# Kernel tuning notes

Measured on AMD Instinct MI355X. Metric: run time of the kernel, lower is better.

## Reference

```python
import jax, jax.numpy as jnp
import numpy as np

N_NODES = 50000
N_EDGES = 1_600_000
F_IN = 32
HIDDEN = 32
HORIZON = 12
K = 2


def setup_inputs() -> dict:
    key = jax.random.key(0)
    ks = jax.random.split(key, 12)
    s = 0.1  # keep gates away from saturation
    x = jax.random.normal(ks[0], (N_NODES, 1, F_IN), dtype=jnp.float32)
    edge_index = jax.random.randint(ks[1], (2, N_EDGES), 0, N_NODES, dtype=jnp.int64)
    edge_weight = jax.random.uniform(ks[2], (N_EDGES,), dtype=jnp.float32)
    Wx = jax.random.normal(ks[3], (4, K, F_IN, HIDDEN), dtype=jnp.float32) * s
    bx = jax.random.normal(ks[4], (4, HIDDEN), dtype=jnp.float32) * s
    Wh = jax.random.normal(ks[5], (4, K, HIDDEN, HIDDEN), dtype=jnp.float32) * s
    bh = jax.random.normal(ks[6], (4, HIDDEN), dtype=jnp.float32) * s
    wc = jax.random.normal(ks[7], (3, HIDDEN), dtype=jnp.float32) * s
    b = jax.random.normal(ks[8], (4, HIDDEN), dtype=jnp.float32) * s
    W_lin = jax.random.normal(ks[9], (HIDDEN, HORIZON), dtype=jnp.float32) * s
    b_lin = jax.random.normal(ks[10], (HORIZON,), dtype=jnp.float32) * s
    h0 = jnp.zeros((N_NODES, HIDDEN), dtype=jnp.float32)
    c0 = jnp.zeros((N_NODES, HIDDEN), dtype=jnp.float32)
    return dict(x=x, edge_index=edge_index, edge_weight=edge_weight, Wx=Wx, bx=bx,
                Wh=Wh, bh=bh, wc=wc, b=b, W_lin=W_lin, b_lin=b_lin, h0=h0, c0=c0)


def reference(x, edge_index, edge_weight, Wx, bx, Wh, bh, wc, b, W_lin, b_lin, h0, c0):
    N = x.shape[0]
    src, dst = edge_index[0], edge_index[1]
    # ChebConv sym normalization with lambda_max=2: L_hat = L - I = -D^{-1/2} A D^{-1/2}
    deg = jax.ops.segment_sum(edge_weight, src, num_segments=N)
    dinv = jnp.where(deg > 0, jax.lax.rsqrt(deg), 0.0)
    nw = -dinv[src] * edge_weight * dinv[dst]  # [E]

    X = x[:, 0, :]  # squeeze(1) -> [N, F]

    def cheb(Z, W, bb):
        # K=2 Chebyshev: T0(Z)=Z, T1(Z)=L_hat Z (sparse gather-scatter)
        LZ = jax.ops.segment_sum(nw[:, None] * Z[src], dst, num_segments=N)
        return Z @ W[0] + LZ @ W[1] + bb

    # gate order: i, f, c, o
    I = jax.nn.sigmoid(cheb(X, Wx[0], bx[0]) + cheb(h0, Wh[0], bh[0]) + wc[0] * c0 + b[0])
    Fg = jax.nn.sigmoid(cheb(X, Wx[1], bx[1]) + cheb(h0, Wh[1], bh[1]) + wc[1] * c0 + b[1])
    T = jnp.tanh(cheb(X, Wx[2], bx[2]) + cheb(h0, Wh[2], bh[2]) + b[2])
    C = Fg * c0 + I * T
    O = jax.nn.sigmoid(cheb(X, Wx[3], bx[3]) + cheb(h0, Wh[3], bh[3]) + wc[2] * C + b[3])
    H = O * jnp.tanh(C)

    h = jax.nn.relu(H) @ W_lin + b_lin  # Linear(32, horizon)
    return (h, H, C)
```

## Files before the change

### kernel.cpp

```cpp
#include <hip/hip_runtime.h>
#include <math.h>

#define HID 32
#define HOR 12
#define NB 256
#define NPT 4

__device__ __forceinline__ float sigmoidf_(float x) { return 1.0f / (1.0f + expf(-x)); }


__global__ __launch_bounds__(256) void k_hist(const int* __restrict__ src,
                                              const int* __restrict__ dst,
                                              int* __restrict__ hist,
                                              int E, int chunk, int ng) {
    __shared__ int hS[256], hD[256];
    int t = threadIdx.x, b = blockIdx.x;
    hS[t] = 0; hD[t] = 0;
    __syncthreads();
    int beg = b * chunk, end = min(E, beg + chunk);
    for (int e = beg + t; e < end; e += 256) {
        atomicAdd(&hS[src[e] >> 8], 1);
        atomicAdd(&hD[dst[e] >> 8], 1);
    }
    __syncthreads();
    if (t < ng) {
        hist[(size_t)t * NB + b] = hS[t];
        hist[((size_t)ng + t) * NB + b] = hD[t];
    }
}

__global__ __launch_bounds__(256) void k_binscan(const int* __restrict__ hist,
                                                 int* __restrict__ off,
                                                 int* __restrict__ binTot, int ng) {
    __shared__ int s[256];
    int b2 = blockIdx.x, t = threadIdx.x;
    int v = hist[(size_t)b2 * NB + t];
    s[t] = v;
    __syncthreads();
    for (int o = 1; o < 256; o <<= 1) {
        int x = (t >= o) ? s[t - o] : 0;
        __syncthreads();
        s[t] += x;
        __syncthreads();
    }
    off[(size_t)b2 * NB + t] = s[t] - v;
    if (t == 255) {
        int idx = (b2 < ng) ? b2 : 256 + (b2 - ng);
        binTot[idx] = s[255];
    }
}

__global__ __launch_bounds__(512) void k_binbase(const int* __restrict__ binTot,
                                                 int* __restrict__ baseS, int* __restrict__ baseD,
                                                 int* __restrict__ rowptr,
                                                 int E, int ng, int N) {
    __shared__ int buf[512];
    int t = threadIdx.x;
    int lt = t & 255;
    int sum = (lt < ng) ? binTot[(t < 256 ? 0 : 256) + lt] : 0;
    buf[t] = sum;
    __syncthreads();
    for (int o = 1; o < 256; o <<= 1) {
        int v = (lt >= o) ? buf[t - o] : 0;
        __syncthreads();
        buf[t] += v;
        __syncthreads();
    }
    int base = buf[t] - sum;
    if (lt < ng) { if (t < 256) baseS[lt] = base; else baseD[lt] = base; }
    if (t == 0)   { baseS[ng] = E; rowptr[N] = E; }
    if (t == 256) { baseD[ng] = E; }
}

__global__ __launch_bounds__(256) void k_scatter(const int* __restrict__ src,
                                                 const int* __restrict__ dst,
                                                 const float* __restrict__ w,
                                                 const int* __restrict__ off,
                                                 const int* __restrict__ baseS,
                                                 const int* __restrict__ baseD,
                                                 int2* __restrict__ tmpS, int2* __restrict__ tmpD,
                                                 int E, int chunk, int ng) {
    __shared__ int cS[256], cD[256];
    int t = threadIdx.x, b = blockIdx.x;
    if (t < ng) {
        cS[t] = off[(size_t)t * NB + b] + baseS[t];
        cD[t] = off[((size_t)ng + t) * NB + b] + baseD[t];
    }
    __syncthreads();
    int beg = b * chunk, end = min(E, beg + chunk);
    for (int e = beg + t; e < end; e += 256) {
        int s = src[e], d = dst[e];
        int wb = __float_as_int(w[e]);
        int pS = atomicAdd(&cS[s >> 8], 1);
        tmpS[pS] = make_int2(s, wb);
        int pD = atomicAdd(&cD[d >> 8], 1);
        tmpD[pD] = make_int2(s | ((d & 255) << 16), wb);
    }
}

__global__ __launch_bounds__(256) void k_degsum(const int2* __restrict__ tmpS,
                                                const int* __restrict__ baseS,
                                                float* __restrict__ dinv, int N) {
    __shared__ float h[256];
    int g = blockIdx.x, t = threadIdx.x;
    h[t] = 0.0f;
    __syncthreads();
    int beg = baseS[g], end = baseS[g + 1];
    for (int i = beg + t; i < end; i += 256) {
        int2 p = tmpS[i];
        atomicAdd(&h[p.x & 255], __int_as_float(p.y));
    }
    __syncthreads();
    int n = (g << 8) + t;
    if (n < N) { float s = h[t]; dinv[n] = (s > 0.0f) ? rsqrtf(s) : 0.0f; }
}

__global__ __launch_bounds__(256) void k_scatter2(const int2* __restrict__ tmpD,
                                                  const int* __restrict__ baseD,
                                                  const float* __restrict__ dinv,
                                                  int* __restrict__ rowptr,
                                                  int2* __restrict__ epair, int N) {
    __shared__ int h[256];
    __shared__ int cur[256];
    int g = blockIdx.x, t = threadIdx.x;
    h[t] = 0;
    __syncthreads();
    int beg = baseD[g], end = baseD[g + 1];
    for (int i = beg + t; i < end; i += 256) atomicAdd(&h[(tmpD[i].x >> 16) & 255], 1);
    __syncthreads();
    int v = h[t];
    for (int off = 1; off < 256; off <<= 1) {
        int x = (t >= off) ? h[t - off] : 0;
        __syncthreads();
        h[t] += x;
        __syncthreads();
    }
    int excl = h[t] - v;
    int n = (g << 8) + t;
    if (n < N) rowptr[n] = beg + excl;
    cur[t] = beg + excl;
    __syncthreads();
    for (int i = beg + t; i < end; i += 256) {
        int2 p = tmpD[i];
        int low = (p.x >> 16) & 255;
        int s = p.x & 0xFFFF;
        int pos = atomicAdd(&cur[low], 1);
        float nw = -dinv[s] * __int_as_float(p.y) * dinv[(g << 8) + low];
        epair[pos] = make_int2(s, __float_as_int(nw));
    }
}

__global__ void k_flags(const float* __restrict__ h0, const float* __restrict__ c0,
                        int* __restrict__ flag, int total) {
    int i = blockIdx.x * 256 + threadIdx.x;
    float a = (i < total) ? h0[i] : 0.0f;
    float c = (i < total) ? c0[i] : 0.0f;
    unsigned long long ba = __ballot(a != 0.0f);
    unsigned long long bc = __ballot(c != 0.0f);
    if ((threadIdx.x & 63) == 0) {
        int m = (ba ? 1 : 0) | (bc ? 2 : 0);
        if (m) atomicOr(flag, m);
    }
}

__global__ __launch_bounds__(256) void k_gather(const int* __restrict__ rowptr,
                                                const int2* __restrict__ epair,
                                                const float* __restrict__ X,
                                                const float* __restrict__ H0,
                                                const int* __restrict__ hflag,
                                                float* __restrict__ LX, float* __restrict__ LH,
                                                int N) {
    int tid = blockIdx.x * 256 + threadIdx.x;
    int n = tid >> 5;
    int f = tid & 31;
    if (n >= N) return;
    int beg = rowptr[n], end = rowptr[n + 1];
    float acc = 0.0f, accH = 0.0f;
    int fl = *hflag;
    if (fl & 1) {
        #pragma unroll 4
        for (int i = beg; i < end; ++i) {
            int2 p = epair[i];
            float w = __int_as_float(p.y);
            acc  += w * X[(p.x << 5) + f];
            accH += w * H0[(p.x << 5) + f];
        }
    } else {
        #pragma unroll 4
        for (int i = beg; i < end; ++i) {
            int2 p = epair[i];
            acc += __int_as_float(p.y) * X[(p.x << 5) + f];
        }
    }
    LX[(n << 5) + f] = acc;
    if (fl & 1) LH[(n << 5) + f] = accH;
}

__global__ __launch_bounds__(256) void k_gates(
    const float* __restrict__ X, const float* __restrict__ LX,
    const float* __restrict__ H0, const float* __restrict__ LH,
    const float* __restrict__ C0,
    const float* __restrict__ Wx, const float* __restrict__ bx,
    const float* __restrict__ Wh, const float* __restrict__ bh,
    const float* __restrict__ wc, const float* __restrict__ b,
    const int* __restrict__ flag,
    float* __restrict__ outH, float* __restrict__ outC, int N) {
    int tid = blockIdx.x * 256 + threadIdx.x;
    int g = tid >> 5;
    int j = tid & 31;
    int n0 = g * NPT;
    if (n0 >= N) return;
    int cnt = min(NPT, N - n0);
    int f2 = *flag;

    if (f2 == 0) {
        float xk[NPT], lxk[NPT];
        #pragma unroll
        for (int i = 0; i < NPT; ++i) { xk[i] = 0.0f; lxk[i] = 0.0f; }
        for (int i = 0; i < cnt; ++i) {
            int base = (n0 + i) << 5;
            xk[i]  = X[base + j];
            lxk[i] = LX[base + j];
        }
        float p0[NPT], p2[NPT], p3[NPT];
        float b0 = bx[0 * HID + j] + bh[0 * HID + j] + b[0 * HID + j];
        float b2 = bx[2 * HID + j] + bh[2 * HID + j] + b[2 * HID + j];
        float b3 = bx[3 * HID + j] + bh[3 * HID + j] + b[3 * HID + j];
        #pragma unroll
        for (int i = 0; i < NPT; ++i) { p0[i] = b0; p2[i] = b2; p3[i] = b3; }

        #pragma unroll 4
        for (int k = 0; k < HID; ++k) {
            int row = k * HID + j;
            float w00 = Wx[0 * 2048 + row], w01 = Wx[0 * 2048 + 1024 + row];
            float w20 = Wx[2 * 2048 + row], w21 = Wx[2 * 2048 + 1024 + row];
            float w30 = Wx[3 * 2048 + row], w31 = Wx[3 * 2048 + 1024 + row];
            #pragma unroll
            for (int i = 0; i < NPT; ++i) {
                float xv  = __shfl(xk[i],  k, 32);
                float lxv = __shfl(lxk[i], k, 32);
                p0[i] += xv * w00 + lxv * w01;
                p2[i] += xv * w20 + lxv * w21;
                p3[i] += xv * w30 + lxv * w31;
            }
        }

        float wc2 = wc[2 * HID + j];
        for (int i = 0; i < cnt; ++i) {
            int base = (n0 + i) << 5;
            float I = sigmoidf_(p0[i]);
            float T = tanhf(p2[i]);
            float C = I * T;
            float O = sigmoidf_(p3[i] + wc2 * C);
            outH[base + j] = O * tanhf(C);
            outC[base + j] = C;
        }
        return;
    }

    float xk[NPT], lxk[NPT], hk[NPT], lhk[NPT];
    #pragma unroll
    for (int i = 0; i < NPT; ++i) { xk[i] = 0.0f; lxk[i] = 0.0f; hk[i] = 0.0f; lhk[i] = 0.0f; }
    for (int i = 0; i < cnt; ++i) {
        int base = (n0 + i) << 5;
        xk[i]  = X[base + j];
        lxk[i] = LX[base + j];
        hk[i]  = H0[base + j];
        lhk[i] = (f2 & 1) ? LH[base + j] : 0.0f;
    }

    float pre[4][NPT];
    #pragma unroll
    for (int gt = 0; gt < 4; ++gt) {
        float bb = bx[gt * HID + j] + bh[gt * HID + j] + b[gt * HID + j];
        #pragma unroll
        for (int i = 0; i < NPT; ++i) pre[gt][i] = bb;
    }

    #pragma unroll 2
    for (int k = 0; k < HID; ++k) {
        float w0[4], w1[4], w2[4], w3[4];
        int row = k * HID + j;
        #pragma unroll
        for (int gt = 0; gt < 4; ++gt) {
            w0[gt] = Wx[gt * 2048 + row];
            w1[gt] = Wx[gt * 2048 + 1024 + row];
            w2[gt] = Wh[gt * 2048 + row];
            w3[gt] = Wh[gt * 2048 + 1024 + row];
        }
        #pragma unroll
        for (int i = 0; i < NPT; ++i) {
            float xv  = __shfl(xk[i],  k, 32);
            float lxv = __shfl(lxk[i], k, 32);
            float hv  = __shfl(hk[i],  k, 32);
            float lhv = __shfl(lhk[i], k, 32);
            #pragma unroll
            for (int gt = 0; gt < 4; ++gt)
                pre[gt][i] += xv * w0[gt] + lxv * w1[gt] + hv * w2[gt] + lhv * w3[gt];
        }
    }

    float wc0 = wc[0 * HID + j], wc1 = wc[1 * HID + j], wc2 = wc[2 * HID + j];
    for (int i = 0; i < cnt; ++i) {
        int base = (n0 + i) << 5;
        float c0v = C0[base + j];
        float I  = sigmoidf_(pre[0][i] + wc0 * c0v);
        float Fg = sigmoidf_(pre[1][i] + wc1 * c0v);
        float T  = tanhf(pre[2][i]);
        float C  = Fg * c0v + I * T;
        float O  = sigmoidf_(pre[3][i] + wc2 * C);
        float H  = O * tanhf(C);
        outH[base + j] = H;
        outC[base + j] = C;
    }
}

__global__ void k_head(const float* __restrict__ H, const float* __restrict__ Wl,
                       const float* __restrict__ bl, float* __restrict__ hout, int N) {
    int tid = blockIdx.x * 256 + threadIdx.x;
    int n = tid / HOR;
    int t = tid - n * HOR;
    if (n >= N) return;
    float acc = bl[t];
    #pragma unroll
    for (int k = 0; k < HID; ++k) {
        float v = H[(n << 5) + k];
        acc += fmaxf(v, 0.0f) * Wl[k * HOR + t];
    }
    hout[n * HOR + t] = acc;
}

extern "C" void kernel_launch(void* const* d_in, const int* in_sizes, int n_in,
                              void* d_out, int out_size, void* d_ws, size_t ws_size,
                              hipStream_t stream) {
    const float* x  = (const float*)d_in[0];
    const int*   ei = (const int*)d_in[1];
    const float* ew = (const float*)d_in[2];
    const float* Wx = (const float*)d_in[3];
    const float* bx = (const float*)d_in[4];
    const float* Wh = (const float*)d_in[5];
    const float* bh = (const float*)d_in[6];
    const float* wc = (const float*)d_in[7];
    const float* b  = (const float*)d_in[8];
    const float* Wl = (const float*)d_in[9];
    const float* bl = (const float*)d_in[10];
    const float* h0 = (const float*)d_in[11];
    const float* c0 = (const float*)d_in[12];

    int N = in_sizes[0] / HID;
    int E = in_sizes[2];
    const int* src = ei;
    const int* dst = ei + E;

    int ng = (N + 255) >> 8;
    int chunk = (E + NB - 1) / NB;

    int* wsi = (int*)d_ws;
    int2*  tmpD   = (int2*)wsi;
    int2*  tmpS   = (int2*)(wsi + 2 * (size_t)E);
    int2*  epair  = tmpS;
    float* LX     = (float*)(wsi + 4 * (size_t)E);
    float* LH     = LX + (size_t)N * HID;
    int*   rowptr = (int*)(LH + (size_t)N * HID);
    int*   hist   = rowptr + (N + 1);
    int*   off    = hist + 2 * (size_t)ng * NB;
    int*   binTot = off + 2 * (size_t)ng * NB;
    int*   baseS  = binTot + 512;
    int*   baseD  = baseS + 257;
    float* dinv   = (float*)(baseD + 257);
    int*   flag   = (int*)(dinv + N);

    float* hOut = (float*)d_out;
    float* HOut = hOut + (size_t)N * HOR;
    float* COut = HOut + (size_t)N * HID;

    hipMemsetAsync(flag, 0, sizeof(int), stream);

    k_hist<<<NB, 256, 0, stream>>>(src, dst, hist, E, chunk, ng);
    k_binscan<<<2 * ng, 256, 0, stream>>>(hist, off, binTot, ng);
    k_binbase<<<1, 512, 0, stream>>>(binTot, baseS, baseD, rowptr, E, ng, N);
    k_scatter<<<NB, 256, 0, stream>>>(src, dst, ew, off, baseS, baseD, tmpS, tmpD, E, chunk, ng);
    k_degsum<<<ng, 256, 0, stream>>>(tmpS, baseS, dinv, N);
    k_flags<<<(N * HID + 255) / 256, 256, 0, stream>>>(h0, c0, flag, N * HID);
    k_scatter2<<<ng, 256, 0, stream>>>(tmpD, baseD, dinv, rowptr, epair, N);

    k_gather<<<(N * HID + 255) / 256, 256, 0, stream>>>(rowptr, epair, x, h0, flag, LX, LH, N);

    int gThreads = ((N + NPT - 1) / NPT) * 32;
    k_gates<<<(gThreads + 255) / 256, 256, 0, stream>>>(x, LX, h0, LH, c0,
                                                        Wx, bx, Wh, bh, wc, b, flag,
                                                        HOut, COut, N);

    k_head<<<(N * HOR + 255) / 256, 256, 0, stream>>>(HOut, Wl, bl, hOut, N);
}
```

Baseline: 278.4 us.

## Shrink CSR bucket width to 64 nodes and transpose offset layout

Changes the CSR build's coarse bucket size from 256 to 64 nodes, giving about 782 buckets instead of 196. The degree-sum and second-scatter kernels therefore launch four times as many blocks, and each block handles fewer edges. Histogram and scatter blocks grow to 1024 threads, the bin-base scan splits into two 1024-thread blocks, and the offset array is transposed so each scatter block reads its offsets contiguously. The aim is more parallelism and less per-block serial work in the edge sort, at the cost of larger histograms, more shared-memory atomics spread over bins, and mostly idle threads in the 256-thread blocks that now cover only 64 nodes.

Result: no change. 275.5 us (-1.0%).

```diff
diff --git a/kernel.cpp b/kernel.cpp
--- a/kernel.cpp
+++ b/kernel.cpp
@@ -3,35 +3,37 @@
 
 #define HID 32
 #define HOR 12
-#define NB 256
+#define NB  256
+#define GSH 6
+#define GW  64
 #define NPT 4
 
 __device__ __forceinline__ float sigmoidf_(float x) { return 1.0f / (1.0f + expf(-x)); }
 
 
-__global__ __launch_bounds__(256) void k_hist(const int* __restrict__ src,
-                                              const int* __restrict__ dst,
-                                              int* __restrict__ hist,
-                                              int E, int chunk, int ng) {
-    __shared__ int hS[256], hD[256];
+__global__ __launch_bounds__(1024) void k_hist(const int* __restrict__ src,
+                                               const int* __restrict__ dst,
+                                               int* __restrict__ hist,
+                                               int E, int chunk, int ng) {
+    __shared__ int hS[1024], hD[1024];
     int t = threadIdx.x, b = blockIdx.x;
-    hS[t] = 0; hD[t] = 0;
+    for (int i = t; i < ng; i += 1024) { hS[i] = 0; hD[i] = 0; }
     __syncthreads();
     int beg = b * chunk, end = min(E, beg + chunk);
-    for (int e = beg + t; e < end; e += 256) {
-        atomicAdd(&hS[src[e] >> 8], 1);
-        atomicAdd(&hD[dst[e] >> 8], 1);
-    }
-    __syncthreads();
-    if (t < ng) {
-        hist[(size_t)t * NB + b] = hS[t];
-        hist[((size_t)ng + t) * NB + b] = hD[t];
+    for (int e = beg + t; e < end; e += 1024) {
+        atomicAdd(&hS[src[e] >> GSH], 1);
+        atomicAdd(&hD[dst[e] >> GSH], 1);
+    }
+    __syncthreads();
+    for (int i = t; i < ng; i += 1024) {
+        hist[(size_t)i * NB + b] = hS[i];
+        hist[((size_t)ng + i) * NB + b] = hD[i];
     }
 }
 
 __global__ __launch_bounds__(256) void k_binscan(const int* __restrict__ hist,
                                                  int* __restrict__ off,
-                                                 int* __restrict__ binTot, int ng) {
+                                                 int* __restrict__ binTot, int ng2) {
     __shared__ int s[256];
     int b2 = blockIdx.x, t = threadIdx.x;
     int v = hist[(size_t)b2 * NB + t];
@@ -43,76 +45,74 @@
         s[t] += x;
         __syncthreads();
     }
-    off[(size_t)b2 * NB + t] = s[t] - v;
-    if (t == 255) {
-        int idx = (b2 < ng) ? b2 : 256 + (b2 - ng);
-        binTot[idx] = s[255];
-    }
-}
-
-__global__ __launch_bounds__(512) void k_binbase(const int* __restrict__ binTot,
-                                                 int* __restrict__ baseS, int* __restrict__ baseD,
-                                                 int* __restrict__ rowptr,
-                                                 int E, int ng, int N) {
-    __shared__ int buf[512];
+    off[(size_t)t * ng2 + b2] = s[t] - v;
+    if (t == 255) binTot[b2] = s[255];
+}
+
+__global__ __launch_bounds__(1024) void k_binbase(const int* __restrict__ binTot,
+                                                  int* __restrict__ baseS, int* __restrict__ baseD,
+                                                  int* __restrict__ rowptr,
+                                                  int E, int ng, int N) {
+    __shared__ int buf[1024];
     int t = threadIdx.x;
-    int lt = t & 255;
-    int sum = (lt < ng) ? binTot[(t < 256 ? 0 : 256) + lt] : 0;
+    int isD = blockIdx.x;
+    int sum = (t < ng) ? binTot[isD * ng + t] : 0;
     buf[t] = sum;
     __syncthreads();
-    for (int o = 1; o < 256; o <<= 1) {
-        int v = (lt >= o) ? buf[t - o] : 0;
+    for (int o = 1; o < 1024; o <<= 1) {
+        int v = (t >= o) ? buf[t - o] : 0;
         __syncthreads();
         buf[t] += v;
         __syncthreads();
     }
     int base = buf[t] - sum;
-    if (lt < ng) { if (t < 256) baseS[lt] = base; else baseD[lt] = base; }
-    if (t == 0)   { baseS[ng] = E; rowptr[N] = E; }
-    if (t == 256) { baseD[ng] = E; }
-}
-
-__global__ __launch_bounds__(256) void k_scatter(const int* __restrict__ src,
-                                                 const int* __restrict__ dst,
-                                                 const float* __restrict__ w,
-                                                 const int* __restrict__ off,
-                                                 const int* __restrict__ baseS,
-                                                 const int* __restrict__ baseD,
-                                                 int2* __restrict__ tmpS, int2* __restrict__ tmpD,
-                                                 int E, int chunk, int ng) {
-    __shared__ int cS[256], cD[256];
+    int* B = isD ? baseD : baseS;
+    if (t < ng) B[t] = base;
+    if (t == 0) { B[ng] = E; if (!isD) rowptr[N] = E; }
+}
+
+__global__ __launch_bounds__(1024) void k_scatter(const int* __restrict__ src,
+                                                  const int* __restrict__ dst,
+                                                  const float* __restrict__ w,
+                                                  const int* __restrict__ off,
+                                                  const int* __restrict__ baseS,
+                                                  const int* __restrict__ baseD,
+                                                  int2* __restrict__ tmpS, int2* __restrict__ tmpD,
+                                                  int E, int chunk, int ng) {
+    __shared__ int cS[1024], cD[1024];
     int t = threadIdx.x, b = blockIdx.x;
-    if (t < ng) {
-        cS[t] = off[(size_t)t * NB + b] + baseS[t];
-        cD[t] = off[((size_t)ng + t) * NB + b] + baseD[t];
+    int ng2 = 2 * ng;
+    for (int i = t; i < ng; i += 1024) {
+        cS[i] = off[(size_t)b * ng2 + i] + baseS[i];
+        cD[i] = off[(size_t)b * ng2 + ng + i] + baseD[i];
     }
     __syncthreads();
     int beg = b * chunk, end = min(E, beg + chunk);
-    for (int e = beg + t; e < end; e += 256) {
+    for (int e = beg + t; e < end; e += 1024) {
         int s = src[e], d = dst[e];
         int wb = __float_as_int(w[e]);
-        int pS = atomicAdd(&cS[s >> 8], 1);
+        int pS = atomicAdd(&cS[s >> GSH], 1);
         tmpS[pS] = make_int2(s, wb);
-        int pD = atomicAdd(&cD[d >> 8], 1);
-        tmpD[pD] = make_int2(s | ((d & 255) << 16), wb);
+        int pD = atomicAdd(&cD[d >> GSH], 1);
+        tmpD[pD] = make_int2(s | ((d & (GW - 1)) << 16), wb);
     }
 }
 
 __global__ __launch_bounds__(256) void k_degsum(const int2* __restrict__ tmpS,
                                                 const int* __restrict__ baseS,
                                                 float* __restrict__ dinv, int N) {
-    __shared__ float h[256];
+    __shared__ float h[GW];
     int g = blockIdx.x, t = threadIdx.x;
-    h[t] = 0.0f;
+    if (t < GW) h[t] = 0.0f;
     __syncthreads();
     int beg = baseS[g], end = baseS[g + 1];
     for (int i = beg + t; i < end; i += 256) {
         int2 p = tmpS[i];
-        atomicAdd(&h[p.x & 255], __int_as_float(p.y));
-    }
-    __syncthreads();
-    int n = (g << 8) + t;
-    if (n < N) { float s = h[t]; dinv[n] = (s > 0.0f) ? rsqrtf(s) : 0.0f; }
+        atomicAdd(&h[p.x & (GW - 1)], __int_as_float(p.y));
+    }
+    __syncthreads();
+    int n = (g << GSH) + t;
+    if (t < GW && n < N) { float s = h[t]; dinv[n] = (s > 0.0f) ? rsqrtf(s) : 0.0f; }
 }
 
 __global__ __launch_bounds__(256) void k_scatter2(const int2* __restrict__ tmpD,
@@ -120,32 +120,33 @@
                                                   const float* __restrict__ dinv,
                                                   int* __restrict__ rowptr,
                                                   int2* __restrict__ epair, int N) {
-    __shared__ int h[256];
-    __shared__ int cur[256];
+    __shared__ int h[GW], cur[GW];
     int g = blockIdx.x, t = threadIdx.x;
-    h[t] = 0;
+    if (t < GW) h[t] = 0;
     __syncthreads();
     int beg = baseD[g], end = baseD[g + 1];
-    for (int i = beg + t; i < end; i += 256) atomicAdd(&h[(tmpD[i].x >> 16) & 255], 1);
-    __syncthreads();
-    int v = h[t];
-    for (int off = 1; off < 256; off <<= 1) {
-        int x = (t >= off) ? h[t - off] : 0;
-        __syncthreads();
-        h[t] += x;
-        __syncthreads();
-    }
-    int excl = h[t] - v;
-    int n = (g << 8) + t;
-    if (n < N) rowptr[n] = beg + excl;
-    cur[t] = beg + excl;
+    for (int i = beg + t; i < end; i += 256) atomicAdd(&h[(tmpD[i].x >> 16) & (GW - 1)], 1);
+    __syncthreads();
+    int v = (t < GW) ? h[t] : 0;
+    for (int o = 1; o < GW; o <<= 1) {
+        int x = (t < GW && t >= o) ? h[t - o] : 0;
+        __syncthreads();
+        if (t < GW && t >= o) h[t] += x;
+        __syncthreads();
+    }
+    if (t < GW) {
+        int excl = h[t] - v;
+        int n = (g << GSH) + t;
+        if (n < N) rowptr[n] = beg + excl;
+        cur[t] = beg + excl;
+    }
     __syncthreads();
     for (int i = beg + t; i < end; i += 256) {
         int2 p = tmpD[i];
-        int low = (p.x >> 16) & 255;
+        int low = (p.x >> 16) & (GW - 1);
         int s = p.x & 0xFFFF;
         int pos = atomicAdd(&cur[low], 1);
-        float nw = -dinv[s] * __int_as_float(p.y) * dinv[(g << 8) + low];
+        float nw = -dinv[s] * __int_as_float(p.y) * dinv[(g << GSH) + low];
         epair[pos] = make_int2(s, __float_as_int(nw));
     }
 }
@@ -352,7 +353,8 @@
     const int* src = ei;
     const int* dst = ei + E;
 
-    int ng = (N + 255) >> 8;
+    int ng = (N + GW - 1) >> GSH;
+    int ng2 = 2 * ng;
     int chunk = (E + NB - 1) / NB;
 
     int* wsi = (int*)d_ws;
@@ -363,11 +365,11 @@
     float* LH     = LX + (size_t)N * HID;
     int*   rowptr = (int*)(LH + (size_t)N * HID);
     int*   hist   = rowptr + (N + 1);
-    int*   off    = hist + 2 * (size_t)ng * NB;
-    int*   binTot = off + 2 * (size_t)ng * NB;
-    int*   baseS  = binTot + 512;
-    int*   baseD  = baseS + 257;
-    float* dinv   = (float*)(baseD + 257);
+    int*   off    = hist + (size_t)ng2 * NB;
+    int*   binTot = off + (size_t)ng2 * NB;
+    int*   baseS  = binTot + 2048;
+    int*   baseD  = baseS + (ng + 1);
+    float* dinv   = (float*)(baseD + (ng + 1));
     int*   flag   = (int*)(dinv + N);
 
     float* hOut = (float*)d_out;
@@ -376,10 +378,10 @@
 
     hipMemsetAsync(flag, 0, sizeof(int), stream);
 
-    k_hist<<<NB, 256, 0, stream>>>(src, dst, hist, E, chunk, ng);
-    k_binscan<<<2 * ng, 256, 0, stream>>>(hist, off, binTot, ng);
-    k_binbase<<<1, 512, 0, stream>>>(binTot, baseS, baseD, rowptr, E, ng, N);
-    k_scatter<<<NB, 256, 0, stream>>>(src, dst, ew, off, baseS, baseD, tmpS, tmpD, E, chunk, ng);
+    k_hist<<<NB, 1024, 0, stream>>>(src, dst, hist, E, chunk, ng);
+    k_binscan<<<ng2, 256, 0, stream>>>(hist, off, binTot, ng2);
+    k_binbase<<<2, 1024, 0, stream>>>(binTot, baseS, baseD, rowptr, E, ng, N);
+    k_scatter<<<NB, 1024, 0, stream>>>(src, dst, ew, off, baseS, baseD, tmpS, tmpD, E, chunk, ng);
     k_degsum<<<ng, 256, 0, stream>>>(tmpS, baseS, dinv, N);
     k_flags<<<(N * HID + 255) / 256, 256, 0, stream>>>(h0, c0, flag, N * HID);
     k_scatter2<<<ng, 256, 0, stream>>>(tmpD, baseD, dinv, rowptr, epair, N);
```
